# Kernel tuning notes

Measured on AMD Instinct MI355X. Metric: run time of the kernel, lower is better.

## Reference

```python
import jax, jax.numpy as jnp
import numpy as np

H = 4096          # hidden_size
HS = 64           # head_size
NH = H // HS      # num_heads = 64
TM = 64           # TIME_MIX_EXTRA_DIM (hidden_size == 4096)
TD = 128          # TIME_DECAY_EXTRA_DIM (hidden_size == 4096)
EPS = 1e-5


def _ln(v, w, b):
    mu = v.mean(-1, keepdims=True)
    var = v.var(-1, keepdims=True)
    return (v - mu) / jnp.sqrt(var + EPS) * w + b


def setup_inputs() -> dict:
    key = jax.random.key(0)
    ks = jax.random.split(key, 20)
    def n(i, shape, s=0.02):
        return jax.random.normal(ks[i], shape, dtype=jnp.float32) * s
    return {
        "x": n(0, (1, 1, H), 1.0),
        "state1": n(1, (1, 1, H), 1.0),
        "state2": n(2, (NH, HS, HS), 1.0),
        "ln1_w": jnp.ones((H,), jnp.float32),
        "ln1_b": jnp.zeros((H,), jnp.float32),
        "time_maa_x": n(3, (1, 1, H), 0.1),
        "time_maa": n(4, (5, 1, H), 0.1),       # stacked [w,k,v,r,g] mixes
        "maa_w1": n(5, (H, 5 * TM)),
        "maa_w2": n(6, (5, TM, H)),
        "time_decay": n(7, (NH, HS, 1), 0.5),
        "time_first": n(8, (NH, HS, 1), 0.5),
        "decay_w1": n(9, (H, TD)),
        "decay_w2": n(10, (TD, H)),
        "Wr": n(11, (H, H)),
        "Wk": n(12, (H, H)),
        "Wv": n(13, (H, H)),
        "Wg": n(14, (H, H)),
        "Wo": n(15, (H, H)),
        "lnx_w": jnp.ones((H,), jnp.float32),
        "lnx_b": jnp.zeros((H,), jnp.float32),
    }


def reference(x, state1, state2, ln1_w, ln1_b, time_maa_x, time_maa,
              maa_w1, maa_w2, time_decay, time_first, decay_w1, decay_w2,
              Wr, Wk, Wv, Wg, Wo, lnx_w, lnx_b):
    last_x = x
    xl = _ln(x, ln1_w, ln1_b)                         # [1,1,H]
    sx = state1 - xl                                  # token-shift delta
    xxx = xl + sx * time_maa_x                        # [1,1,H]
    xxx = jnp.tanh(xxx @ maa_w1).reshape(5, 1, TM)    # LoRA down, 5 mixes
    xxx = jnp.einsum('fot,fth->foh', xxx, maa_w2)     # LoRA up -> [5,1,H]
    xxx = xl + sx * (xxx + time_maa)                  # [5,1,H]
    mw, mk, mv, mr, mg = xxx[0], xxx[1], xxx[2], xxx[3], xxx[4]  # each [1,H]

    r = (mr @ Wr.T).reshape(NH, 1, HS)
    k = (mk @ Wk.T).reshape(NH, HS, 1)
    v = (mv @ Wv.T).reshape(NH, 1, HS)
    g = jax.nn.silu(mg @ Wg.T)                        # [1,H]

    # data-dependent decay (LoRA): exp(-exp(clip(w)))
    td = (jnp.tanh(mw @ decay_w1) @ decay_w2).reshape(NH, HS, 1) + time_decay
    td = jnp.exp(-jnp.exp(jnp.clip(td, -9.72, 2.27)))

    kv = k @ v                                        # [NH,HS,HS] outer product
    wkv = kv * time_first + state2                    # bonus + state
    out_h = (r @ wkv).reshape(NH, HS)                 # per-head readout
    state2_out = kv + state2 * td                     # state recurrence

    # InstanceNorm2d over head_size per head (no affine), then elementwise affine
    mu = out_h.mean(-1, keepdims=True)
    var = out_h.var(-1, keepdims=True)
    o = ((out_h - mu) / jnp.sqrt(var + EPS)).reshape(1, 1, H)
    o = o * lnx_w + lnx_b
    o = (o * g) @ Wo.T
    return (last_x + o, xl, state2_out)
```

## Files before the change

### kernel.cpp

```cpp
#include <hip/hip_runtime.h>
#include <hip/hip_bf16.h>


#define HDIM 4096
#define NHEAD 64
#define HSZ 64

#define WS_XL    0
#define WS_SX    4096
#define WS_XXX   8192
#define WS_PART  12288
#define WS_DPART 17408
#define WS_MV    20480
#define WS_TD    40960
#define WS_R     45056
#define WS_K     49152
#define WS_V     53248
#define WS_G     57344
#define WS_OG    61440
#define WS_FLAG  65536

typedef unsigned short bfraw;

__device__ __forceinline__ float bf2f(bfraw u) {
    union { unsigned int u; float f; } v; v.u = ((unsigned int)u) << 16; return v.f;
}
__device__ __forceinline__ bfraw f2bf(float f) {
    union { float f; unsigned int u; } v; v.f = f;
    unsigned int u = v.u;
    unsigned int r = (u + 0x7fffu + ((u >> 16) & 1u)) >> 16;
    return (bfraw)r;
}
__device__ __forceinline__ float ldin(const void* p, long long i, bool isbf) {
    return isbf ? bf2f(((const bfraw*)p)[i]) : ((const float*)p)[i];
}
__device__ __forceinline__ void stout(void* p, long long i, float v, bool isbf) {
    if (isbf) ((bfraw*)p)[i] = f2bf(v); else ((float*)p)[i] = v;
}
__device__ __forceinline__ float waveReduce(float v) {
    for (int m = 32; m; m >>= 1) v += __shfl_xor(v, m);
    return v;
}

__global__ __launch_bounds__(64)
void k0_detect(const void* x, float* ws) {
    int lane = threadIdx.x;
    const bfraw* p = (const bfraw*)x;
    int cnt = 0;
    for (int k = 0; k < 4; ++k) {
        bfraw u = p[lane * 4 + k];
        int e = (u >> 7) & 0xFF;
        if (e >= 96 && e <= 144) cnt++;
    }
    for (int m = 32; m; m >>= 1) cnt += __shfl_xor(cnt, m);
    if (lane == 0) ws[WS_FLAG] = (cnt >= 208) ? 1.0f : 0.0f;
}

__global__ __launch_bounds__(256)
void k1_ln_mix(const void* __restrict__ x, const void* __restrict__ st1,
               const void* __restrict__ lnw, const void* __restrict__ lnb,
               const void* __restrict__ tmx, void* __restrict__ dout,
               float* __restrict__ ws) {
    bool isbf = ws[WS_FLAG] != 0.0f;
    int tid = threadIdx.x;
    float xv[16];
    float s1 = 0.f, s2 = 0.f;
    for (int k = 0; k < 16; ++k) {
        float v = ldin(x, tid + k * 256, isbf);
        xv[k] = v; s1 += v; s2 += v * v;
    }
    s1 = waveReduce(s1); s2 = waveReduce(s2);
    __shared__ float red[8];
    int wid = tid >> 6, lane = tid & 63;
    if (lane == 0) { red[wid] = s1; red[4 + wid] = s2; }
    __syncthreads();
    float t1 = red[0] + red[1] + red[2] + red[3];
    float t2 = red[4] + red[5] + red[6] + red[7];
    float mu = t1 * (1.0f / HDIM);
    float var = fmaxf(t2 * (1.0f / HDIM) - mu * mu, 0.0f);
    float rstd = rsqrtf(var + 1e-5f);
    for (int k = 0; k < 16; ++k) {
        int i = tid + k * 256;
        float xl = (xv[k] - mu) * rstd * ldin(lnw, i, isbf) + ldin(lnb, i, isbf);
        float sx = ldin(st1, i, isbf) - xl;
        float xxx = xl + sx * ldin(tmx, i, isbf);
        stout(dout, 4096 + i, xl, isbf);
        ws[WS_XL + i] = xl;
        ws[WS_SX + i] = sx;
        ws[WS_XXX + i] = xxx;
    }
}

__global__ __launch_bounds__(320)
void k2a_maa_down(const void* __restrict__ w1, float* __restrict__ ws) {
    bool isbf = ws[WS_FLAG] != 0.0f;
    __shared__ float lx[256];
    int tid = threadIdx.x, b = blockIdx.x;
    if (tid < 256) lx[tid] = ws[WS_XXX + b * 256 + tid];
    __syncthreads();
    float acc = 0.f;
    long long base = (long long)b * 256 * 320 + tid;
    #pragma unroll 8
    for (int j = 0; j < 256; ++j) acc += lx[j] * ldin(w1, base + (long long)j * 320, isbf);
    ws[WS_PART + b * 320 + tid] = acc;
}

__global__ __launch_bounds__(256)
void k2c_maa_up(const void* __restrict__ w2, const void* __restrict__ tm,
                float* __restrict__ ws) {
    bool isbf = ws[WS_FLAG] != 0.0f;
    int tid = threadIdx.x;
    int f = blockIdx.x >> 4;
    int hb = (blockIdx.x & 15) << 8;
    __shared__ float zl[64];
    if (tid < 64) {
        float s = 0.f;
        #pragma unroll
        for (int b = 0; b < 16; ++b) s += ws[WS_PART + b * 320 + f * 64 + tid];
        zl[tid] = tanhf(s);
    }
    __syncthreads();
    int h = hb + tid;
    float acc = 0.f;
    long long base = (long long)f * 64 * HDIM + h;
    #pragma unroll 8
    for (int t = 0; t < 64; ++t) acc += zl[t] * ldin(w2, base + (long long)t * HDIM, isbf);
    float mval = ws[WS_XL + h] + ws[WS_SX + h] * (acc + ldin(tm, f * HDIM + h, isbf));
    ws[WS_MV + f * HDIM + h] = mval;
}

__global__ __launch_bounds__(128)
void k3a_decay_down(const void* __restrict__ dw1, float* __restrict__ ws) {
    bool isbf = ws[WS_FLAG] != 0.0f;
    __shared__ float lm[256];
    int tid = threadIdx.x, b = blockIdx.x;
    lm[tid]       = ws[WS_MV + b * 256 + tid];
    lm[tid + 128] = ws[WS_MV + b * 256 + 128 + tid];
    __syncthreads();
    float acc = 0.f;
    long long base = (long long)b * 256 * 128 + tid;
    #pragma unroll 8
    for (int j = 0; j < 256; ++j) acc += lm[j] * ldin(dw1, base + (long long)j * 128, isbf);
    ws[WS_DPART + b * 128 + tid] = acc;
}

__global__ __launch_bounds__(256)
void k3b_decay_up(const void* __restrict__ dw2, const void* __restrict__ tdec,
                  float* __restrict__ ws) {
    bool isbf = ws[WS_FLAG] != 0.0f;
    int tid = threadIdx.x;
    __shared__ float dz[128];
    if (tid < 128) {
        float s = 0.f;
        #pragma unroll
        for (int b = 0; b < 16; ++b) s += ws[WS_DPART + b * 128 + tid];
        dz[tid] = tanhf(s);
    }
    __syncthreads();
    int i = blockIdx.x * 256 + tid;
    float acc = 0.f;
    #pragma unroll 8
    for (int t = 0; t < 128; ++t) acc += dz[t] * ldin(dw2, (long long)t * HDIM + i, isbf);
    float tv = acc + ldin(tdec, i, isbf);
    tv = fminf(fmaxf(tv, -9.72f), 2.27f);
    ws[WS_TD + i] = expf(-expf(tv));
}

__device__ __forceinline__ float dot_row_dual(const void* __restrict__ W, long long row,
                                              const float* __restrict__ m,
                                              int lane, bool isbf) {
    float acc = 0.f;
    if (isbf) {
        const bfraw* wr = (const bfraw*)W + row * HDIM;
        uint4 wv[8];
        #pragma unroll
        for (int it = 0; it < 8; ++it)
            wv[it] = *(const uint4*)(wr + it * 512 + lane * 8);
        #pragma unroll
        for (int it = 0; it < 8; ++it) {
            int base = it * 512 + lane * 8;
            float4 m0 = *(const float4*)(m + base);
            float4 m1 = *(const float4*)(m + base + 4);
            uint4 w4 = wv[it];
            acc += bf2f((bfraw)(w4.x & 0xffff)) * m0.x + bf2f((bfraw)(w4.x >> 16)) * m0.y;
            acc += bf2f((bfraw)(w4.y & 0xffff)) * m0.z + bf2f((bfraw)(w4.y >> 16)) * m0.w;
            acc += bf2f((bfraw)(w4.z & 0xffff)) * m1.x + bf2f((bfraw)(w4.z >> 16)) * m1.y;
            acc += bf2f((bfraw)(w4.w & 0xffff)) * m1.z + bf2f((bfraw)(w4.w >> 16)) * m1.w;
        }
    } else {
        const float* wr = (const float*)W + row * HDIM;
        float4 av[16];
        #pragma unroll
        for (int it = 0; it < 8; ++it) {
            av[2 * it]     = *(const float4*)(wr + it * 512 + lane * 8);
            av[2 * it + 1] = *(const float4*)(wr + it * 512 + lane * 8 + 4);
        }
        #pragma unroll
        for (int it = 0; it < 8; ++it) {
            int base = it * 512 + lane * 8;
            float4 m0 = *(const float4*)(m + base);
            float4 m1 = *(const float4*)(m + base + 4);
            float4 a0 = av[2 * it], a1 = av[2 * it + 1];
            acc += a0.x * m0.x + a0.y * m0.y + a0.z * m0.z + a0.w * m0.w;
            acc += a1.x * m1.x + a1.y * m1.y + a1.z * m1.z + a1.w * m1.w;
        }
    }
    return waveReduce(acc);
}

__global__ __launch_bounds__(256)
void k4_matvec4(const void* __restrict__ Wr, const void* __restrict__ Wk,
                const void* __restrict__ Wv, const void* __restrict__ Wg,
                float* __restrict__ ws) {
    bool isbf = ws[WS_FLAG] != 0.0f;
    int tid = threadIdx.x;
    int wave = tid >> 6, lane = tid & 63;
    int gr = blockIdx.x * 4 + wave;
    int mat = gr >> 12;
    int row = gr & 4095;
    const void* W; const float* m; float* y;
    if (mat == 0)      { W = Wr; m = ws + WS_MV + 3 * HDIM; y = ws + WS_R; }
    else if (mat == 1) { W = Wk; m = ws + WS_MV + 1 * HDIM; y = ws + WS_K; }
    else if (mat == 2) { W = Wv; m = ws + WS_MV + 2 * HDIM; y = ws + WS_V; }
    else               { W = Wg; m = ws + WS_MV + 4 * HDIM; y = ws + WS_G; }
    float acc = dot_row_dual(W, row, m, lane, isbf);
    if (lane == 0) {
        if (mat == 3) acc = acc / (1.0f + expf(-acc));
        y[row] = acc;
    }
}

__global__ __launch_bounds__(64)
void k5_heads(const void* __restrict__ state2, const void* __restrict__ tfirst,
              const void* __restrict__ lnxw, const void* __restrict__ lnxb,
              void* __restrict__ dout, float* __restrict__ ws) {
    bool isbf = ws[WS_FLAG] != 0.0f;
    int h = blockIdx.x, j = threadIdx.x;
    int gi = h * 64 + j;
    float rj = ws[WS_R + gi], kj = ws[WS_K + gi], vj = ws[WS_V + gi];
    float tdj = ws[WS_TD + gi];
    float tfj = ldin(tfirst, gi, isbf);
    __shared__ float lr[64], lk[64], ltd[64];
    lr[j] = rj; lk[j] = kj; ltd[j] = tdj;
    float c = waveReduce(rj * kj * tfj);
    __syncthreads();
    float acc = 0.f;
    long long sbase = (long long)h * 4096 + j;
    #pragma unroll 8
    for (int i = 0; i < 64; ++i) {
        float s = ldin(state2, sbase + i * 64, isbf);
        acc += lr[i] * s;
        stout(dout, 8192 + sbase + i * 64, lk[i] * vj + s * ltd[i], isbf);
    }
    float oh = vj * c + acc;
    float s1 = waveReduce(oh);
    float s2 = waveReduce(oh * oh);
    float mu = s1 * (1.0f / 64.0f);
    float var = fmaxf(s2 * (1.0f / 64.0f) - mu * mu, 0.0f);
    float rstd = rsqrtf(var + 1e-5f);
    float o = (oh - mu) * rstd * ldin(lnxw, gi, isbf) + ldin(lnxb, gi, isbf);
    ws[WS_OG + gi] = o * ws[WS_G + gi];
}

__global__ __launch_bounds__(256)
void k6_out(const void* __restrict__ Wo, const void* __restrict__ x,
            void* __restrict__ dout, float* __restrict__ ws) {
    bool isbf = ws[WS_FLAG] != 0.0f;
    int tid = threadIdx.x;
    int wave = tid >> 6, lane = tid & 63;
    int row = blockIdx.x * 4 + wave;
    float acc = dot_row_dual(Wo, row, ws + WS_OG, lane, isbf);
    if (lane == 0) stout(dout, row, ldin(x, row, isbf) + acc, isbf);
}

extern "C" void kernel_launch(void* const* d_in, const int* in_sizes, int n_in,
                              void* d_out, int out_size, void* d_ws, size_t ws_size,
                              hipStream_t stream) {
    const void* x      = d_in[0];
    const void* st1    = d_in[1];
    const void* st2    = d_in[2];
    const void* ln1w   = d_in[3];
    const void* ln1b   = d_in[4];
    const void* tmx    = d_in[5];
    const void* tmaa   = d_in[6];
    const void* maw1   = d_in[7];
    const void* maw2   = d_in[8];
    const void* tdec   = d_in[9];
    const void* tfirst = d_in[10];
    const void* dw1    = d_in[11];
    const void* dw2    = d_in[12];
    const void* Wr     = d_in[13];
    const void* Wk     = d_in[14];
    const void* Wv     = d_in[15];
    const void* Wg     = d_in[16];
    const void* Wo     = d_in[17];
    const void* lnxw   = d_in[18];
    const void* lnxb   = d_in[19];

    float* ws = (float*)d_ws;

    k0_detect<<<1, 64, 0, stream>>>(x, ws);
    k1_ln_mix<<<1, 256, 0, stream>>>(x, st1, ln1w, ln1b, tmx, d_out, ws);
    k2a_maa_down<<<16, 320, 0, stream>>>(maw1, ws);
    k2c_maa_up<<<80, 256, 0, stream>>>(maw2, tmaa, ws);
    k3a_decay_down<<<16, 128, 0, stream>>>(dw1, ws);
    k3b_decay_up<<<16, 256, 0, stream>>>(dw2, tdec, ws);
    k4_matvec4<<<4096, 256, 0, stream>>>(Wr, Wk, Wv, Wg, ws);
    k5_heads<<<64, 64, 0, stream>>>(st2, tfirst, lnxw, lnxb, d_out, ws);
    k6_out<<<1024, 256, 0, stream>>>(Wo, x, d_out, ws);
}
```

Baseline: 438.6 us.

## Stage mix vectors in LDS, fold detect kernel, widen LoRA grids, swizzle matvec rows

Removes the separate dtype-detect launch by folding it into the layernorm kernel. The LoRA down-projections get more blocks with shorter reductions, and the partial-sum buffers are relocated. The big matvec kernels now stage the input vector in LDS, handle two rows per wave, and use a swizzled block-to-row mapping. The fp32 path uses contiguous float4 loads split into halves with sched barriers, trading extra LDS fill per block for less global traffic on the vector and fewer launches.

```diff
diff --git a/kernel.cpp b/kernel.cpp
--- a/kernel.cpp
+++ b/kernel.cpp
@@ -9,16 +9,16 @@
 #define WS_XL    0
 #define WS_SX    4096
 #define WS_XXX   8192
-#define WS_PART  12288
-#define WS_DPART 17408
-#define WS_MV    20480
-#define WS_TD    40960
-#define WS_R     45056
-#define WS_K     49152
-#define WS_V     53248
-#define WS_G     57344
-#define WS_OG    61440
-#define WS_FLAG  65536
+#define WS_MV    12288
+#define WS_PART  32768
+#define WS_DPART 32768
+#define WS_TD    53248
+#define WS_R     57344
+#define WS_K     61440
+#define WS_V     65536
+#define WS_G     69632
+#define WS_OG    73728
+#define WS_FLAG  77824
 
 typedef unsigned short bfraw;
 
@@ -42,27 +42,32 @@
     return v;
 }
 
-__global__ __launch_bounds__(64)
-void k0_detect(const void* x, float* ws) {
-    int lane = threadIdx.x;
-    const bfraw* p = (const bfraw*)x;
-    int cnt = 0;
-    for (int k = 0; k < 4; ++k) {
-        bfraw u = p[lane * 4 + k];
-        int e = (u >> 7) & 0xFF;
-        if (e >= 96 && e <= 144) cnt++;
-    }
-    for (int m = 32; m; m >>= 1) cnt += __shfl_xor(cnt, m);
-    if (lane == 0) ws[WS_FLAG] = (cnt >= 208) ? 1.0f : 0.0f;
-}
-
 __global__ __launch_bounds__(256)
 void k1_ln_mix(const void* __restrict__ x, const void* __restrict__ st1,
                const void* __restrict__ lnw, const void* __restrict__ lnb,
                const void* __restrict__ tmx, void* __restrict__ dout,
                float* __restrict__ ws) {
-    bool isbf = ws[WS_FLAG] != 0.0f;
-    int tid = threadIdx.x;
+    int tid = threadIdx.x;
+    __shared__ float red[8];
+    __shared__ float sflag;
+    {
+        const bfraw* p = (const bfraw*)x;
+        bfraw u = p[tid];
+        int e = (u >> 7) & 0xFF;
+        int cnt = (e >= 96 && e <= 144) ? 1 : 0;
+        for (int m = 32; m; m >>= 1) cnt += __shfl_xor(cnt, m);
+        if ((tid & 63) == 0) red[tid >> 6] = (float)cnt;
+        __syncthreads();
+        if (tid == 0) {
+            float c = red[0] + red[1] + red[2] + red[3];
+            float fl = (c >= 208.0f) ? 1.0f : 0.0f;
+            sflag = fl;
+            ws[WS_FLAG] = fl;
+        }
+        __syncthreads();
+    }
+    bool isbf = sflag != 0.0f;
+
     float xv[16];
     float s1 = 0.f, s2 = 0.f;
     for (int k = 0; k < 16; ++k) {
@@ -70,7 +75,6 @@
         xv[k] = v; s1 += v; s2 += v * v;
     }
     s1 = waveReduce(s1); s2 = waveReduce(s2);
-    __shared__ float red[8];
     int wid = tid >> 6, lane = tid & 63;
     if (lane == 0) { red[wid] = s1; red[4 + wid] = s2; }
     __syncthreads();
@@ -94,14 +98,14 @@
 __global__ __launch_bounds__(320)
 void k2a_maa_down(const void* __restrict__ w1, float* __restrict__ ws) {
     bool isbf = ws[WS_FLAG] != 0.0f;
-    __shared__ float lx[256];
+    __shared__ float lx[64];
     int tid = threadIdx.x, b = blockIdx.x;
-    if (tid < 256) lx[tid] = ws[WS_XXX + b * 256 + tid];
-    __syncthreads();
-    float acc = 0.f;
-    long long base = (long long)b * 256 * 320 + tid;
-    #pragma unroll 8
-    for (int j = 0; j < 256; ++j) acc += lx[j] * ldin(w1, base + (long long)j * 320, isbf);
+    if (tid < 64) lx[tid] = ws[WS_XXX + b * 64 + tid];
+    __syncthreads();
+    float acc = 0.f;
+    long long base = (long long)b * 64 * 320 + tid;
+    #pragma unroll 8
+    for (int j = 0; j < 64; ++j) acc += lx[j] * ldin(w1, base + (long long)j * 320, isbf);
     ws[WS_PART + b * 320 + tid] = acc;
 }
 
@@ -115,8 +119,8 @@
     __shared__ float zl[64];
     if (tid < 64) {
         float s = 0.f;
-        #pragma unroll
-        for (int b = 0; b < 16; ++b) s += ws[WS_PART + b * 320 + f * 64 + tid];
+        #pragma unroll 8
+        for (int b = 0; b < 64; ++b) s += ws[WS_PART + b * 320 + f * 64 + tid];
         zl[tid] = tanhf(s);
     }
     __syncthreads();
@@ -132,32 +136,31 @@
 __global__ __launch_bounds__(128)
 void k3a_decay_down(const void* __restrict__ dw1, float* __restrict__ ws) {
     bool isbf = ws[WS_FLAG] != 0.0f;
-    __shared__ float lm[256];
+    __shared__ float lm[32];
     int tid = threadIdx.x, b = blockIdx.x;
-    lm[tid]       = ws[WS_MV + b * 256 + tid];
-    lm[tid + 128] = ws[WS_MV + b * 256 + 128 + tid];
-    __syncthreads();
-    float acc = 0.f;
-    long long base = (long long)b * 256 * 128 + tid;
-    #pragma unroll 8
-    for (int j = 0; j < 256; ++j) acc += lm[j] * ldin(dw1, base + (long long)j * 128, isbf);
+    if (tid < 32) lm[tid] = ws[WS_MV + b * 32 + tid];
+    __syncthreads();
+    float acc = 0.f;
+    long long base = (long long)b * 32 * 128 + tid;
+    #pragma unroll 8
+    for (int j = 0; j < 32; ++j) acc += lm[j] * ldin(dw1, base + (long long)j * 128, isbf);
     ws[WS_DPART + b * 128 + tid] = acc;
 }
 
-__global__ __launch_bounds__(256)
+__global__ __launch_bounds__(128)
 void k3b_decay_up(const void* __restrict__ dw2, const void* __restrict__ tdec,
                   float* __restrict__ ws) {
     bool isbf = ws[WS_FLAG] != 0.0f;
     int tid = threadIdx.x;
     __shared__ float dz[128];
-    if (tid < 128) {
+    {
         float s = 0.f;
-        #pragma unroll
-        for (int b = 0; b < 16; ++b) s += ws[WS_DPART + b * 128 + tid];
+        #pragma unroll 8
+        for (int b = 0; b < 128; ++b) s += ws[WS_DPART + b * 128 + tid];
         dz[tid] = tanhf(s);
     }
     __syncthreads();
-    int i = blockIdx.x * 256 + tid;
+    int i = blockIdx.x * 128 + tid;
     float acc = 0.f;
     #pragma unroll 8
     for (int t = 0; t < 128; ++t) acc += dz[t] * ldin(dw2, (long long)t * HDIM + i, isbf);
@@ -166,9 +169,9 @@
     ws[WS_TD + i] = expf(-expf(tv));
 }
 
-__device__ __forceinline__ float dot_row_dual(const void* __restrict__ W, long long row,
-                                              const float* __restrict__ m,
-                                              int lane, bool isbf) {
+__device__ __forceinline__ float dot_row_lds(const void* __restrict__ W, long long row,
+                                             const float* __restrict__ mLds,
+                                             int lane, bool isbf) {
     float acc = 0.f;
     if (isbf) {
         const bfraw* wr = (const bfraw*)W + row * HDIM;
@@ -176,11 +179,12 @@
         #pragma unroll
         for (int it = 0; it < 8; ++it)
             wv[it] = *(const uint4*)(wr + it * 512 + lane * 8);
+        __builtin_amdgcn_sched_barrier(0);
         #pragma unroll
         for (int it = 0; it < 8; ++it) {
             int base = it * 512 + lane * 8;
-            float4 m0 = *(const float4*)(m + base);
-            float4 m1 = *(const float4*)(m + base + 4);
+            float4 m0 = *(const float4*)(mLds + base);
+            float4 m1 = *(const float4*)(mLds + base + 4);
             uint4 w4 = wv[it];
             acc += bf2f((bfraw)(w4.x & 0xffff)) * m0.x + bf2f((bfraw)(w4.x >> 16)) * m0.y;
             acc += bf2f((bfraw)(w4.y & 0xffff)) * m0.z + bf2f((bfraw)(w4.y >> 16)) * m0.w;
@@ -189,20 +193,20 @@
         }
     } else {
         const float* wr = (const float*)W + row * HDIM;
-        float4 av[16];
         #pragma unroll
-        for (int it = 0; it < 8; ++it) {
-            av[2 * it]     = *(const float4*)(wr + it * 512 + lane * 8);
-            av[2 * it + 1] = *(const float4*)(wr + it * 512 + lane * 8 + 4);
-        }
-        #pragma unroll
-        for (int it = 0; it < 8; ++it) {
-            int base = it * 512 + lane * 8;
-            float4 m0 = *(const float4*)(m + base);
-            float4 m1 = *(const float4*)(m + base + 4);
-            float4 a0 = av[2 * it], a1 = av[2 * it + 1];
-            acc += a0.x * m0.x + a0.y * m0.y + a0.z * m0.z + a0.w * m0.w;
-            acc += a1.x * m1.x + a1.y * m1.y + a1.z * m1.z + a1.w * m1.w;
+        for (int h = 0; h < 2; ++h) {
+            float4 av[8];
+            #pragma unroll
+            for (int it = 0; it < 8; ++it)
+                av[it] = *(const float4*)(wr + h * 2048 + it * 256 + lane * 4);
+            __builtin_amdgcn_sched_barrier(0);
+            #pragma unroll
+            for (int it = 0; it < 8; ++it) {
+                int base = h * 2048 + it * 256 + lane * 4;
+                float4 m0 = *(const float4*)(mLds + base);
+                float4 a = av[it];
+                acc += a.x * m0.x + a.y * m0.y + a.z * m0.z + a.w * m0.w;
+            }
         }
     }
     return waveReduce(acc);
@@ -214,19 +218,27 @@
                 float* __restrict__ ws) {
     bool isbf = ws[WS_FLAG] != 0.0f;
     int tid = threadIdx.x;
-    int wave = tid >> 6, lane = tid & 63;
-    int gr = blockIdx.x * 4 + wave;
-    int mat = gr >> 12;
-    int row = gr & 4095;
-    const void* W; const float* m; float* y;
-    if (mat == 0)      { W = Wr; m = ws + WS_MV + 3 * HDIM; y = ws + WS_R; }
-    else if (mat == 1) { W = Wk; m = ws + WS_MV + 1 * HDIM; y = ws + WS_K; }
-    else if (mat == 2) { W = Wv; m = ws + WS_MV + 2 * HDIM; y = ws + WS_V; }
-    else               { W = Wg; m = ws + WS_MV + 4 * HDIM; y = ws + WS_G; }
-    float acc = dot_row_dual(W, row, m, lane, isbf);
-    if (lane == 0) {
-        if (mat == 3) acc = acc / (1.0f + expf(-acc));
-        y[row] = acc;
+    int wid = tid >> 6, lane = tid & 63;
+    int mat = blockIdx.x >> 9;
+    int bb = blockIdx.x & 511;
+    int bs = (bb & 7) * 64 + (bb >> 3);
+    const void* W; const float* msrc; float* y;
+    if (mat == 0)      { W = Wr; msrc = ws + WS_MV + 3 * HDIM; y = ws + WS_R; }
+    else if (mat == 1) { W = Wk; msrc = ws + WS_MV + 1 * HDIM; y = ws + WS_K; }
+    else if (mat == 2) { W = Wv; msrc = ws + WS_MV + 2 * HDIM; y = ws + WS_V; }
+    else               { W = Wg; msrc = ws + WS_MV + 4 * HDIM; y = ws + WS_G; }
+    __shared__ __align__(16) float lm[HDIM];
+    for (int i = tid * 4; i < HDIM; i += 1024)
+        *(float4*)(lm + i) = *(const float4*)(msrc + i);
+    __syncthreads();
+    #pragma unroll
+    for (int k = 0; k < 2; ++k) {
+        int row = bs * 4 + wid + k * 2048;
+        float acc = dot_row_lds(W, row, lm, lane, isbf);
+        if (lane == 0) {
+            if (mat == 3) acc = acc / (1.0f + expf(-acc));
+            y[row] = acc;
+        }
     }
 }
 
@@ -267,10 +279,19 @@
             void* __restrict__ dout, float* __restrict__ ws) {
     bool isbf = ws[WS_FLAG] != 0.0f;
     int tid = threadIdx.x;
-    int wave = tid >> 6, lane = tid & 63;
-    int row = blockIdx.x * 4 + wave;
-    float acc = dot_row_dual(Wo, row, ws + WS_OG, lane, isbf);
-    if (lane == 0) stout(dout, row, ldin(x, row, isbf) + acc, isbf);
+    int wid = tid >> 6, lane = tid & 63;
+    int bb = blockIdx.x;
+    int bs = (bb & 7) * 64 + (bb >> 3);
+    __shared__ __align__(16) float lm[HDIM];
+    for (int i = tid * 4; i < HDIM; i += 1024)
+        *(float4*)(lm + i) = *(const float4*)(ws + WS_OG + i);
+    __syncthreads();
+    #pragma unroll
+    for (int k = 0; k < 2; ++k) {
+        int row = bs * 4 + wid + k * 2048;
+        float acc = dot_row_lds(Wo, row, lm, lane, isbf);
+        if (lane == 0) stout(dout, row, ldin(x, row, isbf) + acc, isbf);
+    }
 }
 
 extern "C" void kernel_launch(void* const* d_in, const int* in_sizes, int n_in,
@@ -299,13 +320,12 @@
 
     float* ws = (float*)d_ws;
 
-    k0_detect<<<1, 64, 0, stream>>>(x, ws);
     k1_ln_mix<<<1, 256, 0, stream>>>(x, st1, ln1w, ln1b, tmx, d_out, ws);
-    k2a_maa_down<<<16, 320, 0, stream>>>(maw1, ws);
+    k2a_maa_down<<<64, 320, 0, stream>>>(maw1, ws);
     k2c_maa_up<<<80, 256, 0, stream>>>(maw2, tmaa, ws);
-    k3a_decay_down<<<16, 128, 0, stream>>>(dw1, ws);
-    k3b_decay_up<<<16, 256, 0, stream>>>(dw2, tdec, ws);
-    k4_matvec4<<<4096, 256, 0, stream>>>(Wr, Wk, Wv, Wg, ws);
+    k3a_decay_down<<<128, 128, 0, stream>>>(dw1, ws);
+    k3b_decay_up<<<32, 128, 0, stream>>>(dw2, tdec, ws);
+    k4_matvec4<<<2048, 256, 0, stream>>>(Wr, Wk, Wv, Wg, ws);
     k5_heads<<<64, 64, 0, stream>>>(st2, tfirst, lnxw, lnxb, d_out, ws);
-    k6_out<<<1024, 256, 0, stream>>>(Wo, x, d_out, ws);
-}
+    k6_out<<<512, 256, 0, stream>>>(Wo, x, d_out, ws);
+}
```

Result: faster. 416.4 us (-5.1%).
